# Performance work log

Measured on AMD Instinct MI355X. Metric: run time of the kernel, lower is better.

Reference implementation:

```python
import jax, jax.numpy as jnp
import numpy as np
import math

B, N_SEQ, SEQ_LEN, C_M = 1, 256, 256, 256
N_HEADS, C_HIDDEN = 8, 32
HC = N_HEADS * C_HIDDEN
LN_EPS = 1e-5


def setup_inputs() -> dict:
    key = jax.random.key(0)
    ks = jax.random.split(key, 8)
    s_in = 1.0 / math.sqrt(C_M)
    s_out = 1.0 / math.sqrt(HC)
    return {
        "m": jax.random.normal(ks[0], (B, N_SEQ, SEQ_LEN, C_M), dtype=jnp.float32),
        "ln_w": jnp.ones((C_M,), dtype=jnp.float32),
        "ln_b": jnp.zeros((C_M,), dtype=jnp.float32),
        "wq": jax.random.normal(ks[1], (C_M, HC), dtype=jnp.float32) * s_in,
        "wk": jax.random.normal(ks[2], (C_M, HC), dtype=jnp.float32) * s_in,
        "wv": jax.random.normal(ks[3], (C_M, HC), dtype=jnp.float32) * s_in,
        "wg": jax.random.normal(ks[4], (C_M, HC), dtype=jnp.float32) * s_in,
        "bg": jnp.zeros((HC,), dtype=jnp.float32),
        "wo": jax.random.normal(ks[5], (HC, C_M), dtype=jnp.float32) * s_out,
        "bo": jnp.zeros((C_M,), dtype=jnp.float32),
    }


def reference(m, ln_w, ln_b, wq, wk, wv, wg, bg, wo, bo):
    b, s, l, _ = m.shape  # [B, n_seq, seq_len, c_m]
    # LayerNorm over c_m
    mu = jnp.mean(m, axis=-1, keepdims=True)
    var = jnp.mean(jnp.square(m - mu), axis=-1, keepdims=True)
    mn = (m - mu) * jax.lax.rsqrt(var + LN_EPS) * ln_w + ln_b  # [B, S, L, c_m]
    mt = jnp.swapaxes(mn, 1, 2)  # [B, L, S, c_m] -- attend over n_seq per column
    # QKV projections (no bias), split heads: [B, L, H, S, ch]
    def proj(w):
        return jnp.transpose(
            (mt @ w).reshape(b, l, s, N_HEADS, C_HIDDEN), (0, 1, 3, 2, 4)
        )
    q, k, v = proj(wq), proj(wk), proj(wv)
    logits = jnp.einsum("blhsc,blhtc->blhst", q, k) / math.sqrt(C_HIDDEN)
    weights = jax.nn.softmax(logits, axis=-1)
    o = jnp.einsum("blhst,blhtc->blhsc", weights, v)  # [B, L, H, S, ch]
    # Faithful to source: permute(0,2,1,3,4) -> [B, H, L, S, ch], then raw reshape
    o = jnp.transpose(o, (0, 2, 1, 3, 4))
    o = o.reshape(b, s, l, HC)  # data-scrambling reshape, as in source
    # Sigmoid gating on layer-normed input (m.transpose(1,2).transpose(1,2) == mn)
    g = jax.nn.sigmoid(mn @ wg + bg)  # [B, S, L, HC]
    o = g * o
    return o @ wo + bo  # [B, S, L, c_m]
```

## Files before the change

kernel.cpp:

```cpp
#include <hip/hip_runtime.h>

typedef unsigned short u16;
typedef __attribute__((ext_vector_type(8))) short bf16x8;
typedef __attribute__((ext_vector_type(4))) float f32x4;

__device__ __forceinline__ float b2f(u16 u){ return __uint_as_float(((unsigned int)u)<<16); }
__device__ __forceinline__ u16 f2b(float f){
  unsigned int u = __float_as_uint(f);
  u += 0x7fffu + ((u>>16)&1u);
  return (u16)(u>>16);
}

__global__ __launch_bounds__(256) void k_ln(const float* __restrict__ m,
    const float* __restrict__ lw, const float* __restrict__ lb,
    u16* __restrict__ mnb){
  int bx = blockIdx.x;
  int l = bx>>3;
  int s0 = (bx&7)*32 + (threadIdx.x>>6)*8;
  int ln = threadIdx.x&63;
  float4 w = *(const float4*)(lw + ln*4);
  float4 b = *(const float4*)(lb + ln*4);
  #pragma unroll
  for (int i=0;i<8;++i){
    int s = s0 + i;
    float4 x = *(const float4*)(m + ((size_t)s*256 + l)*256 + ln*4);
    float s1 = x.x+x.y+x.z+x.w;
    float s2 = x.x*x.x + x.y*x.y + x.z*x.z + x.w*x.w;
    #pragma unroll
    for (int off=32; off>0; off>>=1){
      s1 += __shfl_xor(s1, off);
      s2 += __shfl_xor(s2, off);
    }
    float mu  = s1*(1.0f/256.0f);
    float inv = rsqrtf(s2*(1.0f/256.0f) - mu*mu + 1e-5f);
    u16 o[4];
    o[0] = f2b((x.x-mu)*inv*w.x + b.x);
    o[1] = f2b((x.y-mu)*inv*w.y + b.y);
    o[2] = f2b((x.z-mu)*inv*w.z + b.z);
    o[3] = f2b((x.w-mu)*inv*w.w + b.w);
    *(ushort4*)(mnb + ((size_t)l*256 + s)*256 + ln*4) = *(ushort4*)o;
  }
}

__global__ __launch_bounds__(256) void k_wprep(
    const float* __restrict__ wq, const float* __restrict__ wk,
    const float* __restrict__ wv, const float* __restrict__ wg,
    const float* __restrict__ wo, u16* __restrict__ WT){
  __shared__ u16 T[16*264];
  int z = blockIdx.y, n0 = blockIdx.x*16, tid = threadIdx.x;
  const float* W = (z==0)?wq:(z==1)?wk:(z==2)?wv:(z==3)?wg:wo;
  int nl = tid&15;
  #pragma unroll
  for (int i=0;i<16;++i){
    int cm = i*16 + (tid>>4);
    T[nl*264 + cm] = f2b(W[(size_t)cm*256 + n0 + nl]);
  }
  __syncthreads();
  int n = tid>>4, cc = (tid&15)*16;
  uint4 a = *(const uint4*)&T[n*264 + cc];
  uint4 c = *(const uint4*)&T[n*264 + cc + 8];
  *(uint4*)&WT[(size_t)z*65536 + (size_t)(n0+n)*256 + cc]     = a;
  *(uint4*)&WT[(size_t)z*65536 + (size_t)(n0+n)*256 + cc + 8] = c;
}

__global__ __launch_bounds__(256,3) void k_fused(const u16* __restrict__ mnb,
    const u16* __restrict__ WT, const float* __restrict__ bg,
    const float* __restrict__ bo, float* __restrict__ outp){
  __shared__ u16 smem[26880];
  u16* QS = smem;
  u16* KS = smem + 10240;
  u16* VT = smem + 18432;
  u16* PB = smem;
  float* OS = (float*)smem;
  u16* GS = smem + 18432;

  int bx = blockIdx.x;
  int l = ((bx&7)<<5) | (bx>>6);
  int h = (bx>>3)&7;
  int tid = threadIdx.x;
  int lane = tid&63, wid = tid>>6, quad = lane>>4, lo = lane&15;
  int m0 = wid*64;
  f32x4 z4 = {0.f,0.f,0.f,0.f};

  const u16* Abase = mnb + (size_t)l*65536;
  const u16* Bq = WT + (size_t)0*65536 + (size_t)h*32*256;
  const u16* Bk = WT + (size_t)1*65536 + (size_t)h*32*256;
  const u16* Bv = WT + (size_t)2*65536 + (size_t)h*32*256;
  f32x4 acc[4][6];
  #pragma unroll
  for (int a=0;a<4;++a)
    #pragma unroll
    for (int b=0;b<6;++b) acc[a][b]=z4;

  for (int ks=0; ks<8; ++ks){
    bf16x8 af[4];
    #pragma unroll
    for (int mt=0; mt<4; ++mt)
      af[mt] = *(const bf16x8*)(Abase + (size_t)(m0+mt*16+lo)*256 + ks*32 + quad*8);
    bf16x8 bq[2], bk2[2], bv2[2];
    #pragma unroll
    for (int c2=0; c2<2; ++c2){
      bq[c2]  = *(const bf16x8*)(Bq + (size_t)(c2*16+lo)*256 + ks*32 + quad*8);
      bk2[c2] = *(const bf16x8*)(Bk + (size_t)(c2*16+lo)*256 + ks*32 + quad*8);
      bv2[c2] = *(const bf16x8*)(Bv + (size_t)(c2*16+lo)*256 + ks*32 + quad*8);
    }
    #pragma unroll
    for (int mt=0; mt<4; ++mt){
      #pragma unroll
      for (int c2=0; c2<2; ++c2){
        acc[mt][0+c2] = __builtin_amdgcn_mfma_f32_16x16x32_bf16(af[mt], bq[c2],  acc[mt][0+c2], 0,0,0);
        acc[mt][2+c2] = __builtin_amdgcn_mfma_f32_16x16x32_bf16(af[mt], bk2[c2], acc[mt][2+c2], 0,0,0);
        acc[mt][4+c2] = __builtin_amdgcn_mfma_f32_16x16x32_bf16(af[mt], bv2[c2], acc[mt][4+c2], 0,0,0);
      }
    }
  }
  #pragma unroll
  for (int mt=0; mt<4; ++mt)
    #pragma unroll
    for (int ntl=0; ntl<2; ++ntl)
      #pragma unroll
      for (int r=0; r<4; ++r){
        int s = m0 + mt*16 + quad*4 + r;
        QS[s*40 + ntl*16+lo] = f2b(acc[mt][0+ntl][r]);
        KS[s*32 + ntl*16+lo] = f2b(acc[mt][2+ntl][r]);
        VT[(ntl*16+lo)*264 + s] = f2b(acc[mt][4+ntl][r]);
      }
  bf16x8 qf[4];
  #pragma unroll
  for (int mt=0; mt<4; ++mt)
    qf[mt] = *(const bf16x8*)&QS[(m0+mt*16+lo)*40 + quad*8];
  __syncthreads();

  const float scale = 0.17677669529663687f;
  float lr[16];
  #pragma unroll
  for (int i=0;i<16;++i) lr[i]=0.f;
  f32x4 o_acc[4][2];
  #pragma unroll
  for (int a=0;a<4;++a){ o_acc[a][0]=z4; o_acc[a][1]=z4; }
  int pbase = wid*64*40;

  for (int ts=0; ts<8; ++ts){
    bf16x8 kf[2];
    #pragma unroll
    for (int ntl=0; ntl<2; ++ntl)
      kf[ntl] = *(const bf16x8*)&KS[(ts*32+ntl*16+lo)*32 + quad*8];
    #pragma unroll
    for (int mt=0; mt<4; ++mt){
      #pragma unroll
      for (int ntl=0; ntl<2; ++ntl){
        f32x4 sa = __builtin_amdgcn_mfma_f32_16x16x32_bf16(qf[mt], kf[ntl], z4, 0,0,0);
        #pragma unroll
        for (int r=0; r<4; ++r){
          float p = __expf(sa[r]*scale);
          lr[mt*4+r] += p;
          PB[pbase + (mt*16+quad*4+r)*40 + ntl*16+lo] = f2b(p);
        }
      }
    }
    bf16x8 vf[2];
    #pragma unroll
    for (int nc=0; nc<2; ++nc)
      vf[nc] = *(const bf16x8*)&VT[(nc*16+lo)*264 + ts*32 + quad*8];
    #pragma unroll
    for (int mt=0; mt<4; ++mt){
      bf16x8 paf = *(const bf16x8*)&PB[pbase + (mt*16+lo)*40 + quad*8];
      #pragma unroll
      for (int nc=0; nc<2; ++nc)
        o_acc[mt][nc] = __builtin_amdgcn_mfma_f32_16x16x32_bf16(paf, vf[nc], o_acc[mt][nc], 0,0,0);
    }
  }
  #pragma unroll
  for (int i=0;i<16;++i){
    float v = lr[i];
    v += __shfl_xor(v, 1);
    v += __shfl_xor(v, 2);
    v += __shfl_xor(v, 4);
    v += __shfl_xor(v, 8);
    lr[i] = 1.0f / v;
  }
  __syncthreads();
  #pragma unroll
  for (int mt=0; mt<4; ++mt)
    #pragma unroll
    for (int nc=0; nc<2; ++nc)
      #pragma unroll
      for (int r=0; r<4; ++r){
        int s = m0 + mt*16 + quad*4 + r;
        int c = nc*16 + lo;
        OS[s*32 + c] = o_acc[mt][nc][r] * lr[mt*4+r];
      }
  __syncthreads();

  int sp  = h*32 + (l>>3);
  int l0p = (l&7)*32;
  int wn0 = wid*64;
  const u16* Gw = WT + (size_t)3*65536;
  f32x4 gacc[2][4];
  #pragma unroll
  for (int a=0;a<2;++a)
    #pragma unroll
    for (int b=0;b<4;++b) gacc[a][b]=z4;
  for (int ks=0; ks<8; ++ks){
    bf16x8 ga[2];
    #pragma unroll
    for (int mt2=0; mt2<2; ++mt2)
      ga[mt2] = *(const bf16x8*)(mnb + ((size_t)(l0p+mt2*16+lo)*256 + sp)*256 + ks*32 + quad*8);
    bf16x8 gb[4];
    #pragma unroll
    for (int nt=0; nt<4; ++nt)
      gb[nt] = *(const bf16x8*)(Gw + (size_t)(wn0+nt*16+lo)*256 + ks*32 + quad*8);
    #pragma unroll
    for (int mt2=0; mt2<2; ++mt2)
      #pragma unroll
      for (int nt=0; nt<4; ++nt)
        gacc[mt2][nt] = __builtin_amdgcn_mfma_f32_16x16x32_bf16(ga[mt2], gb[nt], gacc[mt2][nt], 0,0,0);
  }
  #pragma unroll
  for (int nt=0; nt<4; ++nt){
    int n = wn0 + nt*16 + lo;
    float bgn = bg[n];
    #pragma unroll
    for (int mt2=0; mt2<2; ++mt2)
      #pragma unroll
      for (int r=0; r<4; ++r){
        int j = mt2*16 + quad*4 + r;
        float g = 1.f/(1.f + __expf(-(gacc[mt2][nt][r] + bgn)));
        GS[j*264 + n] = f2b(g * OS[j*256 + n]);
      }
  }
  __syncthreads();

  const u16* Ow = WT + (size_t)4*65536;
  f32x4 pacc[2][4];
  #pragma unroll
  for (int a=0;a<2;++a)
    #pragma unroll
    for (int b=0;b<4;++b) pacc[a][b]=z4;
  for (int ks=0; ks<8; ++ks){
    bf16x8 pa[2];
    #pragma unroll
    for (int mt2=0; mt2<2; ++mt2)
      pa[mt2] = *(const bf16x8*)&GS[(mt2*16+lo)*264 + ks*32 + quad*8];
    bf16x8 pb[4];
    #pragma unroll
    for (int nt=0; nt<4; ++nt)
      pb[nt] = *(const bf16x8*)(Ow + (size_t)(wn0+nt*16+lo)*256 + ks*32 + quad*8);
    #pragma unroll
    for (int mt2=0; mt2<2; ++mt2)
      #pragma unroll
      for (int nt=0; nt<4; ++nt)
        pacc[mt2][nt] = __builtin_amdgcn_mfma_f32_16x16x32_bf16(pa[mt2], pb[nt], pacc[mt2][nt], 0,0,0);
  }
  #pragma unroll
  for (int nt=0; nt<4; ++nt){
    int n = wn0 + nt*16 + lo;
    float bon = bo[n];
    #pragma unroll
    for (int mt2=0; mt2<2; ++mt2)
      #pragma unroll
      for (int r=0; r<4; ++r){
        int j = mt2*16 + quad*4 + r;
        outp[((size_t)sp*256 + l0p + j)*256 + n] = pacc[mt2][nt][r] + bon;
      }
  }
}

extern "C" void kernel_launch(void* const* d_in, const int* in_sizes, int n_in,
                              void* d_out, int out_size, void* d_ws, size_t ws_size,
                              hipStream_t stream){
  const float* m  = (const float*)d_in[0];
  const float* lw = (const float*)d_in[1];
  const float* lb = (const float*)d_in[2];
  const float* wq = (const float*)d_in[3];
  const float* wk = (const float*)d_in[4];
  const float* wv = (const float*)d_in[5];
  const float* wg = (const float*)d_in[6];
  const float* bg = (const float*)d_in[7];
  const float* wo = (const float*)d_in[8];
  const float* bo = (const float*)d_in[9];

  u16* mnb = (u16*)d_ws;
  u16* WT  = mnb + (size_t)16777216;
  float* out = (float*)d_out;

  k_wprep<<<dim3(16,5), 256, 0, stream>>>(wq, wk, wv, wg, wo, WT);
  k_ln   <<<2048,       256, 0, stream>>>(m, lw, lb, mnb);
  k_fused<<<2048,       256, 0, stream>>>(mnb, WT, bg, bo, out);
}
```

Measured before the change: 283.5 us.

## Shrink LDS and registers in fused MSA attention kernel, merge prep kernels

Merges the weight-transpose and LayerNorm kernels into one launch, saving a kernel launch. In the fused kernel, Q/K and V projections are computed in separate passes to cut accumulator registers, and Q and P use a small per-wave scratch buffer. K is stored in a chunked layout, and the gate GEMM and output staging are split into two halves so the OS buffer fits in less LDS. Together these lower shared memory and register use to allow four blocks per CU instead of three. The cost is reading the A tile twice and extra barriers, and bf16 rounding now uses the native cast.

```diff
diff --git a/kernel.cpp b/kernel.cpp
--- a/kernel.cpp
+++ b/kernel.cpp
@@ -4,75 +4,73 @@
 typedef __attribute__((ext_vector_type(8))) short bf16x8;
 typedef __attribute__((ext_vector_type(4))) float f32x4;
 
-__device__ __forceinline__ float b2f(u16 u){ return __uint_as_float(((unsigned int)u)<<16); }
 __device__ __forceinline__ u16 f2b(float f){
-  unsigned int u = __float_as_uint(f);
-  u += 0x7fffu + ((u>>16)&1u);
-  return (u16)(u>>16);
+  __bf16 h = (__bf16)f;
+  return __builtin_bit_cast(u16, h);
 }
 
-__global__ __launch_bounds__(256) void k_ln(const float* __restrict__ m,
+__global__ __launch_bounds__(256) void k_pre(const float* __restrict__ m,
     const float* __restrict__ lw, const float* __restrict__ lb,
-    u16* __restrict__ mnb){
-  int bx = blockIdx.x;
-  int l = bx>>3;
-  int s0 = (bx&7)*32 + (threadIdx.x>>6)*8;
-  int ln = threadIdx.x&63;
-  float4 w = *(const float4*)(lw + ln*4);
-  float4 b = *(const float4*)(lb + ln*4);
-  #pragma unroll
-  for (int i=0;i<8;++i){
-    int s = s0 + i;
-    float4 x = *(const float4*)(m + ((size_t)s*256 + l)*256 + ln*4);
-    float s1 = x.x+x.y+x.z+x.w;
-    float s2 = x.x*x.x + x.y*x.y + x.z*x.z + x.w*x.w;
-    #pragma unroll
-    for (int off=32; off>0; off>>=1){
-      s1 += __shfl_xor(s1, off);
-      s2 += __shfl_xor(s2, off);
-    }
-    float mu  = s1*(1.0f/256.0f);
-    float inv = rsqrtf(s2*(1.0f/256.0f) - mu*mu + 1e-5f);
-    u16 o[4];
-    o[0] = f2b((x.x-mu)*inv*w.x + b.x);
-    o[1] = f2b((x.y-mu)*inv*w.y + b.y);
-    o[2] = f2b((x.z-mu)*inv*w.z + b.z);
-    o[3] = f2b((x.w-mu)*inv*w.w + b.w);
-    *(ushort4*)(mnb + ((size_t)l*256 + s)*256 + ln*4) = *(ushort4*)o;
-  }
-}
-
-__global__ __launch_bounds__(256) void k_wprep(
     const float* __restrict__ wq, const float* __restrict__ wk,
     const float* __restrict__ wv, const float* __restrict__ wg,
-    const float* __restrict__ wo, u16* __restrict__ WT){
+    const float* __restrict__ wo,
+    u16* __restrict__ mnb, u16* __restrict__ WT){
   __shared__ u16 T[16*264];
-  int z = blockIdx.y, n0 = blockIdx.x*16, tid = threadIdx.x;
-  const float* W = (z==0)?wq:(z==1)?wk:(z==2)?wv:(z==3)?wg:wo;
-  int nl = tid&15;
-  #pragma unroll
-  for (int i=0;i<16;++i){
-    int cm = i*16 + (tid>>4);
-    T[nl*264 + cm] = f2b(W[(size_t)cm*256 + n0 + nl]);
-  }
-  __syncthreads();
-  int n = tid>>4, cc = (tid&15)*16;
-  uint4 a = *(const uint4*)&T[n*264 + cc];
-  uint4 c = *(const uint4*)&T[n*264 + cc + 8];
-  *(uint4*)&WT[(size_t)z*65536 + (size_t)(n0+n)*256 + cc]     = a;
-  *(uint4*)&WT[(size_t)z*65536 + (size_t)(n0+n)*256 + cc + 8] = c;
+  int bx = blockIdx.x;
+  int tid = threadIdx.x;
+  if (bx < 2048){
+    int l = bx>>3;
+    int s0 = (bx&7)*32 + (tid>>6)*8;
+    int ln = tid&63;
+    float4 w = *(const float4*)(lw + ln*4);
+    float4 b = *(const float4*)(lb + ln*4);
+    #pragma unroll
+    for (int i=0;i<8;++i){
+      int s = s0 + i;
+      float4 x = *(const float4*)(m + ((size_t)s*256 + l)*256 + ln*4);
+      float s1 = x.x+x.y+x.z+x.w;
+      float s2 = x.x*x.x + x.y*x.y + x.z*x.z + x.w*x.w;
+      #pragma unroll
+      for (int off=32; off>0; off>>=1){
+        s1 += __shfl_xor(s1, off);
+        s2 += __shfl_xor(s2, off);
+      }
+      float mu  = s1*(1.0f/256.0f);
+      float inv = rsqrtf(s2*(1.0f/256.0f) - mu*mu + 1e-5f);
+      u16 o[4];
+      o[0] = f2b((x.x-mu)*inv*w.x + b.x);
+      o[1] = f2b((x.y-mu)*inv*w.y + b.y);
+      o[2] = f2b((x.z-mu)*inv*w.z + b.z);
+      o[3] = f2b((x.w-mu)*inv*w.w + b.w);
+      *(ushort4*)(mnb + ((size_t)l*256 + s)*256 + ln*4) = *(ushort4*)o;
+    }
+  } else {
+    int bb = bx - 2048;
+    int z = bb>>4, n0 = (bb&15)*16;
+    const float* W = (z==0)?wq:(z==1)?wk:(z==2)?wv:(z==3)?wg:wo;
+    int nl = tid&15;
+    #pragma unroll
+    for (int i=0;i<16;++i){
+      int cm = i*16 + (tid>>4);
+      T[nl*264 + cm] = f2b(W[(size_t)cm*256 + n0 + nl]);
+    }
+    __syncthreads();
+    int n = tid>>4, cc = (tid&15)*16;
+    uint4 a = *(const uint4*)&T[n*264 + cc];
+    uint4 c = *(const uint4*)&T[n*264 + cc + 8];
+    *(uint4*)&WT[(size_t)z*65536 + (size_t)(n0+n)*256 + cc]     = a;
+    *(uint4*)&WT[(size_t)z*65536 + (size_t)(n0+n)*256 + cc + 8] = c;
+  }
 }
 
-__global__ __launch_bounds__(256,3) void k_fused(const u16* __restrict__ mnb,
+__global__ __launch_bounds__(256,4) void k_fused(const u16* __restrict__ mnb,
     const u16* __restrict__ WT, const float* __restrict__ bg,
     const float* __restrict__ bo, float* __restrict__ outp){
-  __shared__ u16 smem[26880];
-  u16* QS = smem;
-  u16* KS = smem + 10240;
-  u16* VT = smem + 18432;
-  u16* PB = smem;
+  __shared__ u16 smem[19200];
+  u16* KS2 = smem + 2560;
+  u16* VT  = smem + 10752;
   float* OS = (float*)smem;
-  u16* GS = smem + 18432;
+  u16* GS  = smem + 10752;
 
   int bx = blockIdx.x;
   int l = ((bx&7)<<5) | (bx>>6);
@@ -80,39 +78,76 @@
   int tid = threadIdx.x;
   int lane = tid&63, wid = tid>>6, quad = lane>>4, lo = lane&15;
   int m0 = wid*64;
+  u16* SC = smem + wid*640;
   f32x4 z4 = {0.f,0.f,0.f,0.f};
 
   const u16* Abase = mnb + (size_t)l*65536;
-  const u16* Bq = WT + (size_t)0*65536 + (size_t)h*32*256;
-  const u16* Bk = WT + (size_t)1*65536 + (size_t)h*32*256;
+  const u16* Bq = WT + (size_t)h*32*256;
+  const u16* Bk = WT + (size_t)65536 + (size_t)h*32*256;
   const u16* Bv = WT + (size_t)2*65536 + (size_t)h*32*256;
-  f32x4 acc[4][6];
+
+  f32x4 aqk[4][4];
   #pragma unroll
   for (int a=0;a<4;++a)
     #pragma unroll
-    for (int b=0;b<6;++b) acc[a][b]=z4;
-
+    for (int b=0;b<4;++b) aqk[a][b]=z4;
   for (int ks=0; ks<8; ++ks){
     bf16x8 af[4];
     #pragma unroll
     for (int mt=0; mt<4; ++mt)
       af[mt] = *(const bf16x8*)(Abase + (size_t)(m0+mt*16+lo)*256 + ks*32 + quad*8);
-    bf16x8 bq[2], bk2[2], bv2[2];
+    bf16x8 bq2[2], bk2[2];
     #pragma unroll
     for (int c2=0; c2<2; ++c2){
-      bq[c2]  = *(const bf16x8*)(Bq + (size_t)(c2*16+lo)*256 + ks*32 + quad*8);
+      bq2[c2] = *(const bf16x8*)(Bq + (size_t)(c2*16+lo)*256 + ks*32 + quad*8);
       bk2[c2] = *(const bf16x8*)(Bk + (size_t)(c2*16+lo)*256 + ks*32 + quad*8);
+    }
+    #pragma unroll
+    for (int mt=0; mt<4; ++mt)
+      #pragma unroll
+      for (int c2=0; c2<2; ++c2){
+        aqk[mt][0+c2] = __builtin_amdgcn_mfma_f32_16x16x32_bf16(af[mt], bq2[c2], aqk[mt][0+c2], 0,0,0);
+        aqk[mt][2+c2] = __builtin_amdgcn_mfma_f32_16x16x32_bf16(af[mt], bk2[c2], aqk[mt][2+c2], 0,0,0);
+      }
+  }
+  #pragma unroll
+  for (int mt=0; mt<4; ++mt)
+    #pragma unroll
+    for (int ntl=0; ntl<2; ++ntl)
+      #pragma unroll
+      for (int r=0; r<4; ++r){
+        int t  = m0 + mt*16 + quad*4 + r;
+        int cb = ntl*2 + (lo>>3);
+        KS2[cb*2048 + t*8 + (lo&7)] = f2b(aqk[mt][2+ntl][r]);
+      }
+  bf16x8 qf[4];
+  #pragma unroll
+  for (int mt=0; mt<4; ++mt){
+    #pragma unroll
+    for (int ntl=0; ntl<2; ++ntl)
+      #pragma unroll
+      for (int r=0; r<4; ++r)
+        SC[(quad*4+r)*40 + ntl*16+lo] = f2b(aqk[mt][0+ntl][r]);
+    qf[mt] = *(const bf16x8*)&SC[lo*40 + quad*8];
+  }
+
+  f32x4 av[4][2];
+  #pragma unroll
+  for (int a=0;a<4;++a){ av[a][0]=z4; av[a][1]=z4; }
+  for (int ks=0; ks<8; ++ks){
+    bf16x8 af[4];
+    #pragma unroll
+    for (int mt=0; mt<4; ++mt)
+      af[mt] = *(const bf16x8*)(Abase + (size_t)(m0+mt*16+lo)*256 + ks*32 + quad*8);
+    bf16x8 bv2[2];
+    #pragma unroll
+    for (int c2=0; c2<2; ++c2)
       bv2[c2] = *(const bf16x8*)(Bv + (size_t)(c2*16+lo)*256 + ks*32 + quad*8);
-    }
-    #pragma unroll
-    for (int mt=0; mt<4; ++mt){
-      #pragma unroll
-      for (int c2=0; c2<2; ++c2){
-        acc[mt][0+c2] = __builtin_amdgcn_mfma_f32_16x16x32_bf16(af[mt], bq[c2],  acc[mt][0+c2], 0,0,0);
-        acc[mt][2+c2] = __builtin_amdgcn_mfma_f32_16x16x32_bf16(af[mt], bk2[c2], acc[mt][2+c2], 0,0,0);
-        acc[mt][4+c2] = __builtin_amdgcn_mfma_f32_16x16x32_bf16(af[mt], bv2[c2], acc[mt][4+c2], 0,0,0);
-      }
-    }
+    #pragma unroll
+    for (int mt=0; mt<4; ++mt)
+      #pragma unroll
+      for (int c2=0; c2<2; ++c2)
+        av[mt][c2] = __builtin_amdgcn_mfma_f32_16x16x32_bf16(af[mt], bv2[c2], av[mt][c2], 0,0,0);
   }
   #pragma unroll
   for (int mt=0; mt<4; ++mt)
@@ -120,15 +155,9 @@
     for (int ntl=0; ntl<2; ++ntl)
       #pragma unroll
       for (int r=0; r<4; ++r){
-        int s = m0 + mt*16 + quad*4 + r;
-        QS[s*40 + ntl*16+lo] = f2b(acc[mt][0+ntl][r]);
-        KS[s*32 + ntl*16+lo] = f2b(acc[mt][2+ntl][r]);
-        VT[(ntl*16+lo)*264 + s] = f2b(acc[mt][4+ntl][r]);
-      }
-  bf16x8 qf[4];
-  #pragma unroll
-  for (int mt=0; mt<4; ++mt)
-    qf[mt] = *(const bf16x8*)&QS[(m0+mt*16+lo)*40 + quad*8];
+        int t = m0 + mt*16 + quad*4 + r;
+        VT[(ntl*16+lo)*264 + t] = f2b(av[mt][ntl][r]);
+      }
   __syncthreads();
 
   const float scale = 0.17677669529663687f;
@@ -138,36 +167,32 @@
   f32x4 o_acc[4][2];
   #pragma unroll
   for (int a=0;a<4;++a){ o_acc[a][0]=z4; o_acc[a][1]=z4; }
-  int pbase = wid*64*40;
 
   for (int ts=0; ts<8; ++ts){
     bf16x8 kf[2];
     #pragma unroll
     for (int ntl=0; ntl<2; ++ntl)
-      kf[ntl] = *(const bf16x8*)&KS[(ts*32+ntl*16+lo)*32 + quad*8];
+      kf[ntl] = *(const bf16x8*)&KS2[quad*2048 + (ts*32+ntl*16+lo)*8];
+    bf16x8 vf[2];
+    #pragma unroll
+    for (int nc=0; nc<2; ++nc)
+      vf[nc] = *(const bf16x8*)&VT[(nc*16+lo)*264 + ts*32 + quad*8];
     #pragma unroll
     for (int mt=0; mt<4; ++mt){
-      #pragma unroll
-      for (int ntl=0; ntl<2; ++ntl){
-        f32x4 sa = __builtin_amdgcn_mfma_f32_16x16x32_bf16(qf[mt], kf[ntl], z4, 0,0,0);
+      f32x4 sa[2];
+      sa[0] = __builtin_amdgcn_mfma_f32_16x16x32_bf16(qf[mt], kf[0], z4, 0,0,0);
+      sa[1] = __builtin_amdgcn_mfma_f32_16x16x32_bf16(qf[mt], kf[1], z4, 0,0,0);
+      #pragma unroll
+      for (int ntl=0; ntl<2; ++ntl)
         #pragma unroll
         for (int r=0; r<4; ++r){
-          float p = __expf(sa[r]*scale);
+          float p = __expf(sa[ntl][r]*scale);
           lr[mt*4+r] += p;
-          PB[pbase + (mt*16+quad*4+r)*40 + ntl*16+lo] = f2b(p);
+          SC[(quad*4+r)*40 + ntl*16+lo] = f2b(p);
         }
-      }
-    }
-    bf16x8 vf[2];
-    #pragma unroll
-    for (int nc=0; nc<2; ++nc)
-      vf[nc] = *(const bf16x8*)&VT[(nc*16+lo)*264 + ts*32 + quad*8];
-    #pragma unroll
-    for (int mt=0; mt<4; ++mt){
-      bf16x8 paf = *(const bf16x8*)&PB[pbase + (mt*16+lo)*40 + quad*8];
-      #pragma unroll
-      for (int nc=0; nc<2; ++nc)
-        o_acc[mt][nc] = __builtin_amdgcn_mfma_f32_16x16x32_bf16(paf, vf[nc], o_acc[mt][nc], 0,0,0);
+      bf16x8 paf = *(const bf16x8*)&SC[lo*40 + quad*8];
+      o_acc[mt][0] = __builtin_amdgcn_mfma_f32_16x16x32_bf16(paf, vf[0], o_acc[mt][0], 0,0,0);
+      o_acc[mt][1] = __builtin_amdgcn_mfma_f32_16x16x32_bf16(paf, vf[1], o_acc[mt][1], 0,0,0);
     }
   }
   #pragma unroll
@@ -180,54 +205,88 @@
     lr[i] = 1.0f / v;
   }
   __syncthreads();
-  #pragma unroll
-  for (int mt=0; mt<4; ++mt)
-    #pragma unroll
-    for (int nc=0; nc<2; ++nc)
-      #pragma unroll
-      for (int r=0; r<4; ++r){
-        int s = m0 + mt*16 + quad*4 + r;
-        int c = nc*16 + lo;
-        OS[s*32 + c] = o_acc[mt][nc][r] * lr[mt*4+r];
-      }
-  __syncthreads();
 
   int sp  = h*32 + (l>>3);
   int l0p = (l&7)*32;
   int wn0 = wid*64;
   const u16* Gw = WT + (size_t)3*65536;
-  f32x4 gacc[2][4];
-  #pragma unroll
-  for (int a=0;a<2;++a)
-    #pragma unroll
-    for (int b=0;b<4;++b) gacc[a][b]=z4;
-  for (int ks=0; ks<8; ++ks){
-    bf16x8 ga[2];
-    #pragma unroll
-    for (int mt2=0; mt2<2; ++mt2)
-      ga[mt2] = *(const bf16x8*)(mnb + ((size_t)(l0p+mt2*16+lo)*256 + sp)*256 + ks*32 + quad*8);
+
+  if (wid < 2){
+    #pragma unroll
+    for (int mt=0; mt<4; ++mt)
+      #pragma unroll
+      for (int nc=0; nc<2; ++nc)
+        #pragma unroll
+        for (int r=0; r<4; ++r){
+          int s = m0 + mt*16 + quad*4 + r;
+          OS[s*32 + nc*16+lo] = o_acc[mt][nc][r] * lr[mt*4+r];
+        }
+  }
+  f32x4 gacc0[4];
+  #pragma unroll
+  for (int b=0;b<4;++b) gacc0[b]=z4;
+  for (int ks=0; ks<8; ++ks){
+    bf16x8 ga = *(const bf16x8*)(mnb + ((size_t)(l0p+lo)*256 + sp)*256 + ks*32 + quad*8);
     bf16x8 gb[4];
     #pragma unroll
     for (int nt=0; nt<4; ++nt)
       gb[nt] = *(const bf16x8*)(Gw + (size_t)(wn0+nt*16+lo)*256 + ks*32 + quad*8);
     #pragma unroll
-    for (int mt2=0; mt2<2; ++mt2)
-      #pragma unroll
-      for (int nt=0; nt<4; ++nt)
-        gacc[mt2][nt] = __builtin_amdgcn_mfma_f32_16x16x32_bf16(ga[mt2], gb[nt], gacc[mt2][nt], 0,0,0);
-  }
+    for (int nt=0; nt<4; ++nt)
+      gacc0[nt] = __builtin_amdgcn_mfma_f32_16x16x32_bf16(ga, gb[nt], gacc0[nt], 0,0,0);
+  }
+  __syncthreads();
   #pragma unroll
   for (int nt=0; nt<4; ++nt){
     int n = wn0 + nt*16 + lo;
     float bgn = bg[n];
     #pragma unroll
-    for (int mt2=0; mt2<2; ++mt2)
-      #pragma unroll
-      for (int r=0; r<4; ++r){
-        int j = mt2*16 + quad*4 + r;
-        float g = 1.f/(1.f + __expf(-(gacc[mt2][nt][r] + bgn)));
-        GS[j*264 + n] = f2b(g * OS[j*256 + n]);
-      }
+    for (int r=0; r<4; ++r){
+      int j = quad*4 + r;
+      float g = 1.f/(1.f + __expf(-(gacc0[nt][r] + bgn)));
+      int sidx = j*8 + (n>>5);
+      GS[j*264 + n] = f2b(g * OS[sidx*32 + (n&31)]);
+    }
+  }
+  __syncthreads();
+
+  if (wid >= 2){
+    #pragma unroll
+    for (int mt=0; mt<4; ++mt)
+      #pragma unroll
+      for (int nc=0; nc<2; ++nc)
+        #pragma unroll
+        for (int r=0; r<4; ++r){
+          int s = m0 + mt*16 + quad*4 + r - 128;
+          OS[s*32 + nc*16+lo] = o_acc[mt][nc][r] * lr[mt*4+r];
+        }
+  }
+  f32x4 gacc1[4];
+  #pragma unroll
+  for (int b=0;b<4;++b) gacc1[b]=z4;
+  for (int ks=0; ks<8; ++ks){
+    bf16x8 ga = *(const bf16x8*)(mnb + ((size_t)(l0p+16+lo)*256 + sp)*256 + ks*32 + quad*8);
+    bf16x8 gb[4];
+    #pragma unroll
+    for (int nt=0; nt<4; ++nt)
+      gb[nt] = *(const bf16x8*)(Gw + (size_t)(wn0+nt*16+lo)*256 + ks*32 + quad*8);
+    #pragma unroll
+    for (int nt=0; nt<4; ++nt)
+      gacc1[nt] = __builtin_amdgcn_mfma_f32_16x16x32_bf16(ga, gb[nt], gacc1[nt], 0,0,0);
+  }
+  __syncthreads();
+  #pragma unroll
+  for (int nt=0; nt<4; ++nt){
+    int n = wn0 + nt*16 + lo;
+    float bgn = bg[n];
+    #pragma unroll
+    for (int r=0; r<4; ++r){
+      int jj = quad*4 + r;
+      int j = 16 + jj;
+      float g = 1.f/(1.f + __expf(-(gacc1[nt][r] + bgn)));
+      int sidx = jj*8 + (n>>5);
+      GS[j*264 + n] = f2b(g * OS[sidx*32 + (n&31)]);
+    }
   }
   __syncthreads();
 
@@ -284,7 +343,6 @@
   u16* WT  = mnb + (size_t)16777216;
   float* out = (float*)d_out;
 
-  k_wprep<<<dim3(16,5), 256, 0, stream>>>(wq, wk, wv, wg, wo, WT);
-  k_ln   <<<2048,       256, 0, stream>>>(m, lw, lb, mnb);
-  k_fused<<<2048,       256, 0, stream>>>(mnb, WT, bg, bo, out);
+  k_pre  <<<2128, 256, 0, stream>>>(m, lw, lb, wq, wk, wv, wg, wo, mnb, WT);
+  k_fused<<<2048, 256, 0, stream>>>(mnb, WT, bg, bo, out);
 }
```

New measurement: 355.5 us. +25.4%, slower.

## Write second LN output layout for gate GEMM and merge prep kernels

Applied to the files above, without the earlier changes.

The layernorm kernel now also writes the normalized activations in the original [s,l] order to a second buffer. The gate GEMM reads its A operand from that buffer with contiguous row strides instead of widely strided rows. The weight-prep and layernorm kernels are merged into one launch. The attention inner loop interleaves the score, exp and PV MFMAs per row tile, and bf16 conversion uses the compiler intrinsic. The cost is an extra 32 MB write of bf16 activations and more workspace.

```diff
diff --git a/kernel.cpp b/kernel.cpp
--- a/kernel.cpp
+++ b/kernel.cpp
@@ -4,68 +4,70 @@
 typedef __attribute__((ext_vector_type(8))) short bf16x8;
 typedef __attribute__((ext_vector_type(4))) float f32x4;
 
-__device__ __forceinline__ float b2f(u16 u){ return __uint_as_float(((unsigned int)u)<<16); }
 __device__ __forceinline__ u16 f2b(float f){
-  unsigned int u = __float_as_uint(f);
-  u += 0x7fffu + ((u>>16)&1u);
-  return (u16)(u>>16);
-}
-
-__global__ __launch_bounds__(256) void k_ln(const float* __restrict__ m,
+  __bf16 h = (__bf16)f;
+  return __builtin_bit_cast(u16, h);
+}
+
+__global__ __launch_bounds__(256) void k_pre(const float* __restrict__ m,
     const float* __restrict__ lw, const float* __restrict__ lb,
-    u16* __restrict__ mnb){
-  int bx = blockIdx.x;
-  int l = bx>>3;
-  int s0 = (bx&7)*32 + (threadIdx.x>>6)*8;
-  int ln = threadIdx.x&63;
-  float4 w = *(const float4*)(lw + ln*4);
-  float4 b = *(const float4*)(lb + ln*4);
-  #pragma unroll
-  for (int i=0;i<8;++i){
-    int s = s0 + i;
-    float4 x = *(const float4*)(m + ((size_t)s*256 + l)*256 + ln*4);
-    float s1 = x.x+x.y+x.z+x.w;
-    float s2 = x.x*x.x + x.y*x.y + x.z*x.z + x.w*x.w;
-    #pragma unroll
-    for (int off=32; off>0; off>>=1){
-      s1 += __shfl_xor(s1, off);
-      s2 += __shfl_xor(s2, off);
-    }
-    float mu  = s1*(1.0f/256.0f);
-    float inv = rsqrtf(s2*(1.0f/256.0f) - mu*mu + 1e-5f);
-    u16 o[4];
-    o[0] = f2b((x.x-mu)*inv*w.x + b.x);
-    o[1] = f2b((x.y-mu)*inv*w.y + b.y);
-    o[2] = f2b((x.z-mu)*inv*w.z + b.z);
-    o[3] = f2b((x.w-mu)*inv*w.w + b.w);
-    *(ushort4*)(mnb + ((size_t)l*256 + s)*256 + ln*4) = *(ushort4*)o;
-  }
-}
-
-__global__ __launch_bounds__(256) void k_wprep(
     const float* __restrict__ wq, const float* __restrict__ wk,
     const float* __restrict__ wv, const float* __restrict__ wg,
-    const float* __restrict__ wo, u16* __restrict__ WT){
+    const float* __restrict__ wo,
+    u16* __restrict__ mnb, u16* __restrict__ mnb2, u16* __restrict__ WT){
   __shared__ u16 T[16*264];
-  int z = blockIdx.y, n0 = blockIdx.x*16, tid = threadIdx.x;
-  const float* W = (z==0)?wq:(z==1)?wk:(z==2)?wv:(z==3)?wg:wo;
-  int nl = tid&15;
-  #pragma unroll
-  for (int i=0;i<16;++i){
-    int cm = i*16 + (tid>>4);
-    T[nl*264 + cm] = f2b(W[(size_t)cm*256 + n0 + nl]);
-  }
-  __syncthreads();
-  int n = tid>>4, cc = (tid&15)*16;
-  uint4 a = *(const uint4*)&T[n*264 + cc];
-  uint4 c = *(const uint4*)&T[n*264 + cc + 8];
-  *(uint4*)&WT[(size_t)z*65536 + (size_t)(n0+n)*256 + cc]     = a;
-  *(uint4*)&WT[(size_t)z*65536 + (size_t)(n0+n)*256 + cc + 8] = c;
+  int bx = blockIdx.x;
+  int tid = threadIdx.x;
+  if (bx < 2048){
+    int l = bx>>3;
+    int s0 = (bx&7)*32 + (tid>>6)*8;
+    int ln = tid&63;
+    float4 w = *(const float4*)(lw + ln*4);
+    float4 b = *(const float4*)(lb + ln*4);
+    #pragma unroll
+    for (int i=0;i<8;++i){
+      int s = s0 + i;
+      float4 x = *(const float4*)(m + ((size_t)s*256 + l)*256 + ln*4);
+      float s1 = x.x+x.y+x.z+x.w;
+      float s2 = x.x*x.x + x.y*x.y + x.z*x.z + x.w*x.w;
+      #pragma unroll
+      for (int off=32; off>0; off>>=1){
+        s1 += __shfl_xor(s1, off);
+        s2 += __shfl_xor(s2, off);
+      }
+      float mu  = s1*(1.0f/256.0f);
+      float inv = rsqrtf(s2*(1.0f/256.0f) - mu*mu + 1e-5f);
+      u16 o[4];
+      o[0] = f2b((x.x-mu)*inv*w.x + b.x);
+      o[1] = f2b((x.y-mu)*inv*w.y + b.y);
+      o[2] = f2b((x.z-mu)*inv*w.z + b.z);
+      o[3] = f2b((x.w-mu)*inv*w.w + b.w);
+      *(ushort4*)(mnb  + ((size_t)l*256 + s)*256 + ln*4) = *(ushort4*)o;
+      *(ushort4*)(mnb2 + ((size_t)s*256 + l)*256 + ln*4) = *(ushort4*)o;
+    }
+  } else {
+    int bb = bx - 2048;
+    int z = bb>>4, n0 = (bb&15)*16;
+    const float* W = (z==0)?wq:(z==1)?wk:(z==2)?wv:(z==3)?wg:wo;
+    int nl = tid&15;
+    #pragma unroll
+    for (int i=0;i<16;++i){
+      int cm = i*16 + (tid>>4);
+      T[nl*264 + cm] = f2b(W[(size_t)cm*256 + n0 + nl]);
+    }
+    __syncthreads();
+    int n = tid>>4, cc = (tid&15)*16;
+    uint4 a = *(const uint4*)&T[n*264 + cc];
+    uint4 c = *(const uint4*)&T[n*264 + cc + 8];
+    *(uint4*)&WT[(size_t)z*65536 + (size_t)(n0+n)*256 + cc]     = a;
+    *(uint4*)&WT[(size_t)z*65536 + (size_t)(n0+n)*256 + cc + 8] = c;
+  }
 }
 
 __global__ __launch_bounds__(256,3) void k_fused(const u16* __restrict__ mnb,
-    const u16* __restrict__ WT, const float* __restrict__ bg,
-    const float* __restrict__ bo, float* __restrict__ outp){
+    const u16* __restrict__ mnb2, const u16* __restrict__ WT,
+    const float* __restrict__ bg, const float* __restrict__ bo,
+    float* __restrict__ outp){
   __shared__ u16 smem[26880];
   u16* QS = smem;
   u16* KS = smem + 10240;
@@ -83,8 +85,8 @@
   f32x4 z4 = {0.f,0.f,0.f,0.f};
 
   const u16* Abase = mnb + (size_t)l*65536;
-  const u16* Bq = WT + (size_t)0*65536 + (size_t)h*32*256;
-  const u16* Bk = WT + (size_t)1*65536 + (size_t)h*32*256;
+  const u16* Bq = WT + (size_t)h*32*256;
+  const u16* Bk = WT + (size_t)65536 + (size_t)h*32*256;
   const u16* Bv = WT + (size_t)2*65536 + (size_t)h*32*256;
   f32x4 acc[4][6];
   #pragma unroll
@@ -145,29 +147,26 @@
     #pragma unroll
     for (int ntl=0; ntl<2; ++ntl)
       kf[ntl] = *(const bf16x8*)&KS[(ts*32+ntl*16+lo)*32 + quad*8];
+    bf16x8 vf[2];
+    #pragma unroll
+    for (int nc=0; nc<2; ++nc)
+      vf[nc] = *(const bf16x8*)&VT[(nc*16+lo)*264 + ts*32 + quad*8];
     #pragma unroll
     for (int mt=0; mt<4; ++mt){
-      #pragma unroll
-      for (int ntl=0; ntl<2; ++ntl){
-        f32x4 sa = __builtin_amdgcn_mfma_f32_16x16x32_bf16(qf[mt], kf[ntl], z4, 0,0,0);
+      f32x4 sa[2];
+      sa[0] = __builtin_amdgcn_mfma_f32_16x16x32_bf16(qf[mt], kf[0], z4, 0,0,0);
+      sa[1] = __builtin_amdgcn_mfma_f32_16x16x32_bf16(qf[mt], kf[1], z4, 0,0,0);
+      #pragma unroll
+      for (int ntl=0; ntl<2; ++ntl)
         #pragma unroll
         for (int r=0; r<4; ++r){
-          float p = __expf(sa[r]*scale);
+          float p = __expf(sa[ntl][r]*scale);
           lr[mt*4+r] += p;
           PB[pbase + (mt*16+quad*4+r)*40 + ntl*16+lo] = f2b(p);
         }
-      }
-    }
-    bf16x8 vf[2];
-    #pragma unroll
-    for (int nc=0; nc<2; ++nc)
-      vf[nc] = *(const bf16x8*)&VT[(nc*16+lo)*264 + ts*32 + quad*8];
-    #pragma unroll
-    for (int mt=0; mt<4; ++mt){
       bf16x8 paf = *(const bf16x8*)&PB[pbase + (mt*16+lo)*40 + quad*8];
-      #pragma unroll
-      for (int nc=0; nc<2; ++nc)
-        o_acc[mt][nc] = __builtin_amdgcn_mfma_f32_16x16x32_bf16(paf, vf[nc], o_acc[mt][nc], 0,0,0);
+      o_acc[mt][0] = __builtin_amdgcn_mfma_f32_16x16x32_bf16(paf, vf[0], o_acc[mt][0], 0,0,0);
+      o_acc[mt][1] = __builtin_amdgcn_mfma_f32_16x16x32_bf16(paf, vf[1], o_acc[mt][1], 0,0,0);
     }
   }
   #pragma unroll
@@ -196,6 +195,7 @@
   int l0p = (l&7)*32;
   int wn0 = wid*64;
   const u16* Gw = WT + (size_t)3*65536;
+  const u16* A2 = mnb2 + (size_t)sp*65536;
   f32x4 gacc[2][4];
   #pragma unroll
   for (int a=0;a<2;++a)
@@ -205,7 +205,7 @@
     bf16x8 ga[2];
     #pragma unroll
     for (int mt2=0; mt2<2; ++mt2)
-      ga[mt2] = *(const bf16x8*)(mnb + ((size_t)(l0p+mt2*16+lo)*256 + sp)*256 + ks*32 + quad*8);
+      ga[mt2] = *(const bf16x8*)(A2 + (size_t)(l0p+mt2*16+lo)*256 + ks*32 + quad*8);
     bf16x8 gb[4];
     #pragma unroll
     for (int nt=0; nt<4; ++nt)
@@ -280,11 +280,11 @@
   const float* wo = (const float*)d_in[8];
   const float* bo = (const float*)d_in[9];
 
-  u16* mnb = (u16*)d_ws;
-  u16* WT  = mnb + (size_t)16777216;
+  u16* mnb  = (u16*)d_ws;
+  u16* mnb2 = mnb  + (size_t)16777216;
+  u16* WT   = mnb2 + (size_t)16777216;
   float* out = (float*)d_out;
 
-  k_wprep<<<dim3(16,5), 256, 0, stream>>>(wq, wk, wv, wg, wo, WT);
-  k_ln   <<<2048,       256, 0, stream>>>(m, lw, lb, mnb);
-  k_fused<<<2048,       256, 0, stream>>>(mnb, WT, bg, bo, out);
-}
+  k_pre  <<<2128, 256, 0, stream>>>(m, lw, lb, wq, wk, wv, wg, wo, mnb, mnb2, WT);
+  k_fused<<<2048, 256, 0, stream>>>(mnb, mnb2, WT, bg, bo, out);
+}
```

New measurement: 308.5 us. +8.8%, slower.
